# Kernel optimization log

Hardware: AMD Instinct MI355X
Metric: run time of the kernel (lower is better)

## Reference

```python
import jax, jax.numpy as jnp
import numpy as np

EPS = 1e-07
N, Q = 1368, 21
WS = [16, 32, 64]
ST = [4, 8, 16]
OC = [64, 128, 256]


def _num_pos(n, w, s):
    return int((n - w) / s - EPS) + 1


def setup_inputs() -> dict:
    key = jax.random.key(0)
    kx, k0, k1, k2 = jax.random.split(key, 4)
    B = 64
    x = jax.random.normal(kx, (B, Q, N), dtype=jnp.float32)
    ws = []
    for kk, (w, s, d) in zip([k0, k1, k2], zip(WS, ST, OC)):
        P = _num_pos(N, w, s)
        # xavier-style small init, shape (Nk, q*w) as in FilterbankLinear.weight
        scale = np.sqrt(2.0 / (Q * w + d)).astype(np.float32)
        ws.append(scale * jax.random.normal(kk, (d * P, Q * w), dtype=jnp.float32))
    return {"x": x, "w0": ws[0], "w1": ws[1], "w2": ws[2]}


def _filterbank_linear(x, W, w, s, d):
    # x: (B, q, N); W: (d*P, q*w)
    B, q, n = x.shape
    P = _num_pos(n, w, s)
    # window starts: j*s for j in range(P-1), last window anchored at n-w
    starts = np.concatenate([np.arange(P - 1) * s, np.array([n - w])])
    idx = starts[:, None] + np.arange(w)            # (P, w) static gather indices
    win = x[:, :, idx]                              # (B, q, P, w)
    win = jnp.transpose(win, (0, 2, 1, 3)).reshape(B, P, q * w)  # (B, P, q*w), channel-major like fbank
    h = jnp.einsum('bpf,pdf->bpd', win, W.reshape(P, d, q * w))
    return h.reshape(B, P * d)


def reference(x, w0, w1, w2):
    # FilterbankEdge.forward(x, sample=False): concat of each FilterbankLinear output
    outs = [
        _filterbank_linear(x, W, w, s, d)
        for W, (w, s, d) in zip([w0, w1, w2], zip(WS, ST, OC))
    ]
    return jnp.concatenate(outs, axis=-1)  # (B, 64000)
```

## Files before the change

kernel.cpp:

```cpp
#include <hip/hip_runtime.h>

#define QDIM 21
#define NDIM 1368
#define OUTSTRIDE 64000
#define XTOT (64 * QDIM * NDIM)

typedef __attribute__((ext_vector_type(4))) float f32x4;
typedef __attribute__((ext_vector_type(8))) short bf16x8s;
typedef __attribute__((ext_vector_type(4))) unsigned int u32x4;

typedef __attribute__((address_space(1))) const unsigned int* gas_p;
typedef __attribute__((address_space(3))) unsigned int* las_p;

static __device__ __forceinline__ void gload16(const void* g, char* l) {
    __builtin_amdgcn_global_load_lds((gas_p)g, (las_p)(void*)l, 16, 0, 0);
}

static __device__ __forceinline__ unsigned int pk2(float lo, float hi) {
    unsigned int a = __float_as_uint(lo) + 0x8000u;
    unsigned int b = __float_as_uint(hi) + 0x8000u;
    return __builtin_amdgcn_perm(b, a, 0x07060302);
}

static __device__ __forceinline__ bf16x8s pack8(f32x4 lo, f32x4 hi) {
    u32x4 p;
    p[0] = pk2(lo[0], lo[1]);
    p[1] = pk2(lo[2], lo[3]);
    p[2] = pk2(hi[0], hi[1]);
    p[3] = pk2(hi[2], hi[3]);
    return __builtin_bit_cast(bf16x8s, p);
}

static __device__ __forceinline__ int chunk_swz(int idx, int n) {
    int xcd = idx & 7;
    int i   = idx >> 3;
    int q = n >> 3, r = n & 7;
    int base = (xcd < r) ? xcd * (q + 1) : r * (q + 1) + (xcd - r) * q;
    return base + i;
}

__global__ __launch_bounds__(256)
void xcvt(const float* __restrict__ x, unsigned short* __restrict__ xb) {
    int i = (blockIdx.x * 256 + threadIdx.x) * 8;
    if (i >= XTOT) return;
    f32x4 lo = *(const f32x4*)(x + i);
    f32x4 hi = *(const f32x4*)(x + i + 4);
    *(u32x4*)(xb + i) = __builtin_bit_cast(u32x4, pack8(lo, hi));
}

template<int WLOG2, int NTX, int D, int P, int S, int K, bool ABF16>
__device__ __forceinline__ void fbk_body(const float* __restrict__ x,
                                         const unsigned short* __restrict__ xb,
                                         const float* __restrict__ W,
                                         float* __restrict__ out, int bid,
                                         char* ldsraw) {
    constexpr int WWIN = 1 << WLOG2;
    constexpr int G = (K + 31) / 32;
    constexpr bool TAIL = (K % 32) != 0;
    constexpr int FMAXC = (K - 4) & ~3;
    constexpr int ASTB = ABF16 ? 4096 : 8192;
    constexpr int STB  = ASTB + 8192;
    constexpr int RING = ABF16 ? 3 : 2;

    const int n0 = (bid % NTX) * 64;
    const int p  = bid / NTX;
    const int start = (p == P - 1) ? (NDIM - WWIN) : p * S;

    const int tid  = threadIdx.x;
    const int wid  = tid >> 6;
    const int lane = tid & 63;
    const int wm = (wid >> 1) * 32;
    const int wn = (wid & 1) * 32;
    const int lr = lane & 15;
    const int hi = lane >> 4;
    const int kb = hi * 8;

    const int lrow = lane >> 3;
    const int g4   = ((lane & 7) ^ lrow) * 4;
    const float* Wp  = W + (size_t)(p * D + n0) * K;
    const float* wb0 = Wp + (size_t)(16 * wid + lrow) * K;
    const float* wb1 = wb0 + (size_t)8 * K;
    const int wB = 2048 * wid;

    const unsigned short* xbrow = nullptr;
    if constexpr (ABF16)
        xbrow = xb + (size_t)(16 * wid + (lane >> 2)) * (QDIM * NDIM) + start;
    const float* xb0f = x + (size_t)(16 * wid + lrow) * (QDIM * NDIM) + start;
    const int wA = ABF16 ? (1024 * wid) : (2048 * wid);

    auto STAGE = [&](int t, int sbase) {
        if constexpr (ABF16) {
            int f = t * 32 + (lane & 3) * 8;
            int q = f >> WLOG2;
            int j = f & (WWIN - 1);
            gload16(xbrow + q * NDIM + j, ldsraw + sbase + wA);
        } else {
            int f = t * 32 + g4;
            if constexpr (TAIL) f = (f > FMAXC) ? FMAXC : f;
            int q = f >> WLOG2;
            int j = f & (WWIN - 1);
            const float* ga = xb0f + q * NDIM + j;
            char* la = ldsraw + sbase + wA;
            gload16(ga, la);
            gload16(ga + (size_t)8 * QDIM * NDIM, la + 1024);
        }
        int f = t * 32 + g4;
        if constexpr (TAIL) f = (f > FMAXC) ? FMAXC : f;
        char* lb = ldsraw + sbase + ASTB + wB;
        gload16(wb0 + f, lb);
        gload16(wb1 + f, lb + 1024);
    };

    const int x7 = lr & 7;
    const int c0 = ((hi * 2)     ^ x7) * 16;
    const int c1 = ((hi * 2 + 1) ^ x7) * 16;
    const int oA0b = (wm + lr) * 64 + hi * 16;
    const int oA1b = oA0b + 1024;
    const int oA0 = (wm + lr) * 128;
    const int oA1 = (wm + 16 + lr) * 128;
    const int oB0 = ASTB + (wn + lr) * 128;
    const int oB1 = ASTB + (wn + 16 + lr) * 128;

    f32x4 acc[2][2] = {};

    STAGE(0, 0);
    if constexpr (RING == 3) STAGE(1, STB);

    int cs = 0;
    #pragma unroll 1
    for (int t = 0; t < G; ++t) {
        if constexpr (RING == 3) {
            if (t + 1 < G) { asm volatile("s_waitcnt vmcnt(3)" ::: "memory"); }
            else           { asm volatile("s_waitcnt vmcnt(0)" ::: "memory"); }
        } else {
            asm volatile("s_waitcnt vmcnt(0)" ::: "memory");
        }
        __builtin_amdgcn_sched_barrier(0);
        __builtin_amdgcn_s_barrier();
        __builtin_amdgcn_sched_barrier(0);

        if constexpr (RING == 2) {
            if (t + 1 < G) STAGE(t + 1, cs ^ STB);
            __builtin_amdgcn_sched_barrier(0);
        }

        const char* sb = ldsraw + cs;
        bf16x8s A0, A1;
        if constexpr (ABF16) {
            A0 = *(const bf16x8s*)(sb + oA0b);
            A1 = *(const bf16x8s*)(sb + oA1b);
        } else {
            f32x4 a00 = *(const f32x4*)(sb + oA0 + c0);
            f32x4 a01 = *(const f32x4*)(sb + oA0 + c1);
            f32x4 a10 = *(const f32x4*)(sb + oA1 + c0);
            f32x4 a11 = *(const f32x4*)(sb + oA1 + c1);
            if constexpr (TAIL) {
                if (t == G - 1 && kb >= (K & 31)) {
                    f32x4 z = {0.f, 0.f, 0.f, 0.f};
                    a00 = z; a01 = z; a10 = z; a11 = z;
                }
            }
            A0 = pack8(a00, a01);
            A1 = pack8(a10, a11);
        }
        f32x4 b00 = *(const f32x4*)(sb + oB0 + c0);
        f32x4 b01 = *(const f32x4*)(sb + oB0 + c1);
        f32x4 b10 = *(const f32x4*)(sb + oB1 + c0);
        f32x4 b11 = *(const f32x4*)(sb + oB1 + c1);
        bf16x8s B0 = pack8(b00, b01);
        bf16x8s B1 = pack8(b10, b11);

        acc[0][0] = __builtin_amdgcn_mfma_f32_16x16x32_bf16(A0, B0, acc[0][0], 0, 0, 0);
        acc[0][1] = __builtin_amdgcn_mfma_f32_16x16x32_bf16(A0, B1, acc[0][1], 0, 0, 0);
        acc[1][0] = __builtin_amdgcn_mfma_f32_16x16x32_bf16(A1, B0, acc[1][0], 0, 0, 0);
        acc[1][1] = __builtin_amdgcn_mfma_f32_16x16x32_bf16(A1, B1, acc[1][1], 0, 0, 0);

        __builtin_amdgcn_sched_barrier(0);
        if constexpr (RING == 3) {
            if (t + 2 < G) {
                int pb = (cs == 0) ? 2 * STB : cs - STB;
                STAGE(t + 2, pb);
            }
            cs = (cs == 2 * STB) ? 0 : cs + STB;
        } else {
            cs ^= STB;
        }
    }

    const int colbase = p * D + n0;
    #pragma unroll
    for (int mi = 0; mi < 2; ++mi) {
        #pragma unroll
        for (int ni = 0; ni < 2; ++ni) {
            int col = colbase + wn + ni * 16 + lr;
            int rbase = wm + mi * 16 + hi * 4;
            #pragma unroll
            for (int r = 0; r < 4; ++r) {
                out[(size_t)(rbase + r) * OUTSTRIDE + col] = acc[mi][ni][r];
            }
        }
    }
}

template<bool BF>
__global__ __launch_bounds__(256, 4)
void fbk_fused(const float* __restrict__ x,  const unsigned short* __restrict__ xb,
               const float* __restrict__ w0, const float* __restrict__ w1,
               const float* __restrict__ w2, float* __restrict__ out) {
    __shared__ __align__(16) char ldsraw[36864];
    const int pb = blockIdx.x;
    if (pb < 328) {
        fbk_body<6, 4, 256, 82, 16, 1344, BF>(x, xb, w2, out + 43008, chunk_swz(pb, 328), ldsraw);
    } else if (pb < 662) {
        fbk_body<5, 2, 128, 167, 8, 672, BF>(x, xb, w1, out + 21632, chunk_swz(pb - 328, 334), ldsraw);
    } else {
        fbk_body<4, 1, 64, 338, 4, 336, false>(x, xb, w0, out, chunk_swz(pb - 662, 338), ldsraw);
    }
}

extern "C" void kernel_launch(void* const* d_in, const int* in_sizes, int n_in,
                              void* d_out, int out_size, void* d_ws, size_t ws_size,
                              hipStream_t stream) {
    const float* x  = (const float*)d_in[0];
    const float* w0 = (const float*)d_in[1];
    const float* w1 = (const float*)d_in[2];
    const float* w2 = (const float*)d_in[3];
    float* out = (float*)d_out;
    constexpr size_t XBF_BYTES = (size_t)XTOT * 2;
    if (ws_size >= XBF_BYTES) {
        unsigned short* xbuf = (unsigned short*)d_ws;
        xcvt<<<dim3((XTOT / 8 + 255) / 256), 256, 0, stream>>>(x, xbuf);
        fbk_fused<true><<<dim3(1000), 256, 0, stream>>>(x, xbuf, w0, w1, w2, out);
    } else {
        fbk_fused<false><<<dim3(1000), 256, 0, stream>>>(x, nullptr, w0, w1, w2, out);
    }
}
```

Measured before the change: 45.56 us.

## Halve block tile to 64x32 with 128 threads, 2000 blocks, triple-buffer all paths

Changes the per-block output tile from 64x64 with four waves to 64 rows by 32 columns with two waves, each wave covering 32 rows and all 32 columns. This doubles the grid to 2000 blocks so the GPU has more parallelism and less tail imbalance. The three-stage ring buffer now applies to both the bf16 and fp32 paths. The w0 branch now also uses the bf16 A path, with tail clamping and zero-masking added for K not divisible by 32. Each block reuses x less, so x is re-read more often, and the fp32 path issues more loads per stage.

Measured after the change: 49.71 us. +9.1%, slower.

```diff
diff --git a/kernel.cpp b/kernel.cpp
--- a/kernel.cpp
+++ b/kernel.cpp
@@ -2,8 +2,9 @@
 
 #define QDIM 21
 #define NDIM 1368
+#define QN (QDIM * NDIM)
 #define OUTSTRIDE 64000
-#define XTOT (64 * QDIM * NDIM)
+#define XTOT (64 * QN)
 
 typedef __attribute__((ext_vector_type(4))) float f32x4;
 typedef __attribute__((ext_vector_type(8))) short bf16x8s;
@@ -53,60 +54,58 @@
                                          const unsigned short* __restrict__ xb,
                                          const float* __restrict__ W,
                                          float* __restrict__ out, int bid,
-                                         char* ldsraw) {
+                                         char* lds) {
     constexpr int WWIN = 1 << WLOG2;
     constexpr int G = (K + 31) / 32;
     constexpr bool TAIL = (K % 32) != 0;
+    constexpr int KREM = K & 31;
     constexpr int FMAXC = (K - 4) & ~3;
     constexpr int ASTB = ABF16 ? 4096 : 8192;
-    constexpr int STB  = ASTB + 8192;
-    constexpr int RING = ABF16 ? 3 : 2;
-
-    const int n0 = (bid % NTX) * 64;
+    constexpr int STB  = ASTB + 4096;
+
+    const int n0 = (bid % NTX) * 32;
     const int p  = bid / NTX;
     const int start = (p == P - 1) ? (NDIM - WWIN) : p * S;
 
     const int tid  = threadIdx.x;
     const int wid  = tid >> 6;
     const int lane = tid & 63;
-    const int wm = (wid >> 1) * 32;
-    const int wn = (wid & 1) * 32;
+    const int wm = wid * 32;
     const int lr = lane & 15;
     const int hi = lane >> 4;
     const int kb = hi * 8;
 
     const int lrow = lane >> 3;
     const int g4   = ((lane & 7) ^ lrow) * 4;
-    const float* Wp  = W + (size_t)(p * D + n0) * K;
-    const float* wb0 = Wp + (size_t)(16 * wid + lrow) * K;
+    const float* wb0 = W + (size_t)(p * D + n0 + wid * 16 + lrow) * K;
     const float* wb1 = wb0 + (size_t)8 * K;
-    const int wB = 2048 * wid;
-
-    const unsigned short* xbrow = nullptr;
-    if constexpr (ABF16)
-        xbrow = xb + (size_t)(16 * wid + (lane >> 2)) * (QDIM * NDIM) + start;
-    const float* xb0f = x + (size_t)(16 * wid + lrow) * (QDIM * NDIM) + start;
-    const int wA = ABF16 ? (1024 * wid) : (2048 * wid);
-
-    auto STAGE = [&](int t, int sbase) {
+
+    const unsigned short* xr0 = xb + (size_t)(wid * 32 + (lane >> 2)) * QN + start;
+    const float* xf0 = x + (size_t)(wid * 32 + lrow) * QN + start;
+
+    auto STAGE = [&](int t, int sb) {
         if constexpr (ABF16) {
-            int f = t * 32 + (lane & 3) * 8;
-            int q = f >> WLOG2;
-            int j = f & (WWIN - 1);
-            gload16(xbrow + q * NDIM + j, ldsraw + sbase + wA);
+            int fa = t * 32 + (lane & 3) * 8;
+            if constexpr (TAIL) fa = (fa > K - 8) ? (K - 8) : fa;
+            int qa = fa >> WLOG2, ja = fa & (WWIN - 1);
+            const unsigned short* ga = xr0 + qa * NDIM + ja;
+            char* la = lds + sb + wid * 2048;
+            gload16(ga, la);
+            gload16(ga + (size_t)16 * QN, la + 1024);
         } else {
-            int f = t * 32 + g4;
-            if constexpr (TAIL) f = (f > FMAXC) ? FMAXC : f;
-            int q = f >> WLOG2;
-            int j = f & (WWIN - 1);
-            const float* ga = xb0f + q * NDIM + j;
-            char* la = ldsraw + sbase + wA;
-            gload16(ga, la);
-            gload16(ga + (size_t)8 * QDIM * NDIM, la + 1024);
+            int fa = t * 32 + g4;
+            if constexpr (TAIL) fa = (fa > FMAXC) ? FMAXC : fa;
+            int qa = fa >> WLOG2, ja = fa & (WWIN - 1);
+            const float* ga = xf0 + qa * NDIM + ja;
+            char* la = lds + sb + wid * 4096;
+            gload16(ga,                       la);
+            gload16(ga + (size_t) 8 * QN,     la + 1024);
+            gload16(ga + (size_t)16 * QN,     la + 2048);
+            gload16(ga + (size_t)24 * QN,     la + 3072);
         }
         int f = t * 32 + g4;
         if constexpr (TAIL) f = (f > FMAXC) ? FMAXC : f;
-        char* lb = ldsraw + sbase + ASTB + wB;
+        char* lb = lds + sb + ASTB + wid * 2048;
         gload16(wb0 + f, lb);
         gload16(wb1 + f, lb + 1024);
     };
@@ -115,23 +114,23 @@
     const int c0 = ((hi * 2)     ^ x7) * 16;
     const int c1 = ((hi * 2 + 1) ^ x7) * 16;
     const int oA0b = (wm + lr) * 64 + hi * 16;
-    const int oA1b = oA0b + 1024;
-    const int oA0 = (wm + lr) * 128;
-    const int oA1 = (wm + 16 + lr) * 128;
-    const int oB0 = ASTB + (wn + lr) * 128;
-    const int oB1 = ASTB + (wn + 16 + lr) * 128;
+    const int oA1b = oA0b + 16 * 64;
+    const int oA0f = (wm + lr) * 128;
+    const int oA1f = (wm + 16 + lr) * 128;
+    const int oB0 = ASTB + lr * 128;
+    const int oB1 = ASTB + (16 + lr) * 128;
 
     f32x4 acc[2][2] = {};
 
     STAGE(0, 0);
-    if constexpr (RING == 3) STAGE(1, STB);
+    STAGE(1, STB);
 
     int cs = 0;
     #pragma unroll 1
     for (int t = 0; t < G; ++t) {
-        if constexpr (RING == 3) {
-            if (t + 1 < G) { asm volatile("s_waitcnt vmcnt(3)" ::: "memory"); }
-            else           { asm volatile("s_waitcnt vmcnt(0)" ::: "memory"); }
+        if (t + 1 < G) {
+            if constexpr (ABF16) asm volatile("s_waitcnt vmcnt(4)" ::: "memory");
+            else                 asm volatile("s_waitcnt vmcnt(6)" ::: "memory");
         } else {
             asm volatile("s_waitcnt vmcnt(0)" ::: "memory");
         }
@@ -139,23 +138,24 @@
         __builtin_amdgcn_s_barrier();
         __builtin_amdgcn_sched_barrier(0);
 
-        if constexpr (RING == 2) {
-            if (t + 1 < G) STAGE(t + 1, cs ^ STB);
-            __builtin_amdgcn_sched_barrier(0);
-        }
-
-        const char* sb = ldsraw + cs;
+        const char* sb = lds + cs;
         bf16x8s A0, A1;
         if constexpr (ABF16) {
             A0 = *(const bf16x8s*)(sb + oA0b);
             A1 = *(const bf16x8s*)(sb + oA1b);
+            if constexpr (TAIL) {
+                if (t == G - 1 && kb >= KREM) {
+                    A0 = __builtin_bit_cast(bf16x8s, (u32x4){0u, 0u, 0u, 0u});
+                    A1 = A0;
+                }
+            }
         } else {
-            f32x4 a00 = *(const f32x4*)(sb + oA0 + c0);
-            f32x4 a01 = *(const f32x4*)(sb + oA0 + c1);
-            f32x4 a10 = *(const f32x4*)(sb + oA1 + c0);
-            f32x4 a11 = *(const f32x4*)(sb + oA1 + c1);
+            f32x4 a00 = *(const f32x4*)(sb + oA0f + c0);
+            f32x4 a01 = *(const f32x4*)(sb + oA0f + c1);
+            f32x4 a10 = *(const f32x4*)(sb + oA1f + c0);
+            f32x4 a11 = *(const f32x4*)(sb + oA1f + c1);
             if constexpr (TAIL) {
-                if (t == G - 1 && kb >= (K & 31)) {
+                if (t == G - 1 && kb >= KREM) {
                     f32x4 z = {0.f, 0.f, 0.f, 0.f};
                     a00 = z; a01 = z; a10 = z; a11 = z;
                 }
@@ -176,15 +176,11 @@
         acc[1][1] = __builtin_amdgcn_mfma_f32_16x16x32_bf16(A1, B1, acc[1][1], 0, 0, 0);
 
         __builtin_amdgcn_sched_barrier(0);
-        if constexpr (RING == 3) {
-            if (t + 2 < G) {
-                int pb = (cs == 0) ? 2 * STB : cs - STB;
-                STAGE(t + 2, pb);
-            }
-            cs = (cs == 2 * STB) ? 0 : cs + STB;
-        } else {
-            cs ^= STB;
-        }
+        if (t + 2 < G) {
+            int pb = (cs == 0) ? 2 * STB : cs - STB;
+            STAGE(t + 2, pb);
+        }
+        cs = (cs == 2 * STB) ? 0 : cs + STB;
     }
 
     const int colbase = p * D + n0;
@@ -192,7 +188,7 @@
     for (int mi = 0; mi < 2; ++mi) {
         #pragma unroll
         for (int ni = 0; ni < 2; ++ni) {
-            int col = colbase + wn + ni * 16 + lr;
+            int col = colbase + ni * 16 + lr;
             int rbase = wm + mi * 16 + hi * 4;
             #pragma unroll
             for (int r = 0; r < 4; ++r) {
@@ -203,18 +199,19 @@
 }
 
 template<bool BF>
-__global__ __launch_bounds__(256, 4)
+__global__ __launch_bounds__(128, 3)
 void fbk_fused(const float* __restrict__ x,  const unsigned short* __restrict__ xb,
                const float* __restrict__ w0, const float* __restrict__ w1,
                const float* __restrict__ w2, float* __restrict__ out) {
-    __shared__ __align__(16) char ldsraw[36864];
+    constexpr int STB = BF ? 8192 : 12288;
+    __shared__ __align__(16) char lds[3 * STB];
     const int pb = blockIdx.x;
-    if (pb < 328) {
-        fbk_body<6, 4, 256, 82, 16, 1344, BF>(x, xb, w2, out + 43008, chunk_swz(pb, 328), ldsraw);
-    } else if (pb < 662) {
-        fbk_body<5, 2, 128, 167, 8, 672, BF>(x, xb, w1, out + 21632, chunk_swz(pb - 328, 334), ldsraw);
+    if (pb < 656) {
+        fbk_body<6, 8, 256, 82, 16, 1344, BF>(x, xb, w2, out + 43008, chunk_swz(pb, 656), lds);
+    } else if (pb < 1324) {
+        fbk_body<5, 4, 128, 167, 8, 672, BF>(x, xb, w1, out + 21632, chunk_swz(pb - 656, 668), lds);
     } else {
-        fbk_body<4, 1, 64, 338, 4, 336, false>(x, xb, w0, out, chunk_swz(pb - 662, 338), ldsraw);
+        fbk_body<4, 2, 64, 338, 4, 336, BF>(x, xb, w0, out, chunk_swz(pb - 1324, 676), lds);
     }
 }
 
@@ -230,8 +227,8 @@
     if (ws_size >= XBF_BYTES) {
         unsigned short* xbuf = (unsigned short*)d_ws;
         xcvt<<<dim3((XTOT / 8 + 255) / 256), 256, 0, stream>>>(x, xbuf);
-        fbk_fused<true><<<dim3(1000), 256, 0, stream>>>(x, xbuf, w0, w1, w2, out);
+        fbk_fused<true><<<dim3(2000), 128, 0, stream>>>(x, xbuf, w0, w1, w2, out);
     } else {
-        fbk_fused<false><<<dim3(1000), 256, 0, stream>>>(x, nullptr, w0, w1, w2, out);
-    }
-}
+        fbk_fused<false><<<dim3(2000), 128, 0, stream>>>(x, nullptr, w0, w1, w2, out);
+    }
+}
```
